# Kernel tuning notes

Hardware: AMD Instinct MI355X
Metric: run time of the kernel (lower is better)

Reference implementation:

```python
import jax, jax.numpy as jnp
import numpy as np

T, V, C, G = 65536, 25, 3, 3
H = 32        # GCN hidden channels
OUT = 8       # cfg.STGCN.OUT_FEATURES
LH = 8        # LSTM hidden
DH = 64       # discriminator hidden


def setup_inputs() -> dict:
    key = jax.random.key(0)
    ks = jax.random.split(key, 16)
    def n(i, shape, s=0.3):
        return jax.random.normal(ks[i], shape, dtype=jnp.float32) * s
    A = jax.random.uniform(ks[0], (V, V), dtype=jnp.float32)
    A = A / A.sum(axis=1, keepdims=True)  # row-normalized adjacency
    return dict(
        x=jax.random.normal(ks[1], (1, C, T, V, G), dtype=jnp.float32),
        x0=jax.random.normal(ks[2], (1, 2), dtype=jnp.float32),
        A=A,
        W1=n(3, (H, C)), b1=jnp.zeros((H,), jnp.float32),
        W2=n(4, (OUT, H)), b2=jnp.zeros((OUT,), jnp.float32),
        Wih0=n(5, (4 * LH, 2)), Whh0=n(6, (4 * LH, LH)),
        bih0=jnp.zeros((4 * LH,), jnp.float32), bhh0=jnp.zeros((4 * LH,), jnp.float32),
        Wih1=n(7, (4 * LH, LH)), Whh1=n(8, (4 * LH, LH)),
        bih1=jnp.zeros((4 * LH,), jnp.float32), bhh1=jnp.zeros((4 * LH,), jnp.float32),
        Wfc1=n(9, (8, 32)), bfc1=jnp.zeros((8,), jnp.float32),
        Wfc2=n(10, (2, 8)), bfc2=jnp.zeros((2,), jnp.float32),
        Wd1=n(11, (DH, 32)), bd1=jnp.zeros((DH,), jnp.float32),
        Wd2=n(12, (1, DH)), bd2=jnp.zeros((1,), jnp.float32),
    )


def reference(x, x0, A, W1, b1, W2, b2,
              Wih0, Whh0, bih0, bhh0, Wih1, Whh1, bih1, bhh1,
              Wfc1, bfc1, Wfc2, bfc2, Wd1, bd1, Wd2, bd2):
    Tn = x.shape[2]
    # --- ST-GCN on every (t, group) slice, vectorized over time ---
    g = jnp.transpose(x[0], (1, 3, 0, 2))                       # [T,G,C,V]
    agg = jnp.einsum('tgcv,vu->tgcu', g, A)                     # graph aggregation
    hid = jax.nn.relu(jnp.einsum('hc,tgcu->tghu', W1, agg)
                      + b1[None, None, :, None])                # [T,G,H,V]
    pooled = hid.mean(axis=-1)                                  # global joint pool [T,G,H]
    gout = (jnp.einsum('oh,tgh->tgo', W2, pooled) + b2).reshape(Tn, G * OUT)  # [T,24]
    # --- circle through the 3 group members (joint 5, channels 0/2), faithful formula ---
    px = x[0, 0, :, 5, :]                                       # [T,3]
    py = x[0, 2, :, 5, :]
    x21 = px[:, 1] - px[:, 0]; y21 = py[:, 1] - py[:, 0]
    x32 = px[:, 2] - px[:, 1]; y32 = py[:, 2] - py[:, 1]
    xy21 = px[:, 1] ** 2 - px[:, 0] ** 2 + py[:, 1] ** 2 - py[:, 0] ** 2
    xy32 = px[:, 2] ** 2 - px[:, 1] ** 2 + py[:, 2] ** 2 - py[:, 1] ** 2
    cy = (x32 * xy21 - x21 * xy32) / 2 * (y21 * x32 - y32 * x21)
    cx = (xy21 - 2 * cy * y21) / (2.0 * x21)
    cr = jnp.sqrt((px[:, 0] - cx) ** 2 + (py[:, 0] - cy) ** 2)

    def lstm_cell(inp, h, c, Wih, Whh, bih, bhh):
        gates = Wih @ inp + bih + Whh @ h + bhh
        i, f, gg, o = jnp.split(gates, 4)
        c2 = jax.nn.sigmoid(f) * c + jax.nn.sigmoid(i) * jnp.tanh(gg)
        return jax.nn.sigmoid(o) * jnp.tanh(c2), c2

    # Re-running the LSTM from zero init over the growing traj and taking the last
    # output (as the torch code does) == stepping the LSTM incrementally.
    def step(carry, xs):
        h0, c0, h1, c1, pt = carry
        go, rx, ry, rr = xs
        h0, c0 = lstm_cell(pt, h0, c0, Wih0, Whh0, bih0, bhh0)
        h1, c1 = lstm_cell(h0, h1, c1, Wih1, Whh1, bih1, bhh1)
        state = jnp.concatenate([h1, go])                       # [32]
        reward = jax.nn.sigmoid(Wd2 @ jnp.tanh(Wd1 @ state + bd1) + bd2)
        nxt = Wfc2 @ (Wfc1 @ state + bfc1) + bfc2               # [2]
        dis = jnp.sqrt((nxt[0] - rx) ** 2 + (nxt[1] - ry) ** 2)
        mask = (dis < rr).astype(jnp.int32)
        return (h0, c0, h1, c1, nxt), (state, nxt, reward, mask)

    z = jnp.zeros((LH,), jnp.float32)
    carry0 = (z, z, z, z, x0.reshape(2))
    xs = (gout[:Tn - 1], cx[:Tn - 1], cy[:Tn - 1], cr[:Tn - 1])
    _, (states, nxts, rewards, masks) = jax.lax.scan(step, carry0, xs)
    traj = jnp.concatenate([x0.reshape(1, 2), nxts], axis=0)    # [T,2]
    return states, traj, rewards, masks
```

## Files before the change

kernel.cpp:

```cpp
#include <hip/hip_runtime.h>
#include <math.h>

#define TT 65536
#define NS 65535
#define VV 25
#define CC 3
#define GG 3
#define HH 32
#define OO 8

#define CHUNK 32
#define NCHUNK 2048
#define WARM 64

#define OFF_WC    0
#define OFF_BC    64
#define OFF_W0H1  128
#define OFF_W1T   384
#define OFF_AT    512
#define OFF_PSCAN 1280

#define OUT_STATES 0
#define OUT_TRAJ   (NS*32)
#define OUT_REW    (OUT_TRAJ + TT*2)
#define OUT_MASK   (OUT_REW + NS)

__device__ __forceinline__ float fsigm(float x){ return 1.0f/(1.0f+__expf(-x)); }
__device__ __forceinline__ float ftanh(float x){ return 2.0f/(1.0f+__expf(-2.0f*x)) - 1.0f; }

#define QP(x, k) __int_as_float(__builtin_amdgcn_update_dpp(0, __float_as_int(x), (k)*0x55, 0xF, 0xF, true))
#define RDL(x, l) __int_as_float(__builtin_amdgcn_readlane(__float_as_int(x), (l)))

__device__ __forceinline__ void pkfma_s(float2& acc, float2 w, float2 h){
  asm("v_pk_fma_f32 %0, %1, %2, %0" : "+v"(acc) : "v"(w), "s"(h));
}
__device__ __forceinline__ void pkmul_s(float2& d, float2 w, float2 h){
  asm("v_pk_mul_f32 %0, %1, %2" : "=v"(d) : "v"(w), "s"(h));
}
__device__ __forceinline__ void pkfma_sv(float2& d, float2 w, float2 p, float2 add){
  asm("v_pk_fma_f32 %0, %1, %2, %3" : "=v"(d) : "v"(w), "s"(p), "v"(add));
}
__device__ __forceinline__ float2 pkadd_v(float2 a, float2 b){
  float2 d; asm("v_pk_add_f32 %0, %1, %2" : "=v"(d) : "v"(a), "v"(b)); return d;
}
__device__ __forceinline__ void pkmul_vv(float2& d, float2 a, float2 b){
  asm("v_pk_mul_f32 %0, %1, %2" : "=v"(d) : "v"(a), "v"(b));
}
__device__ __forceinline__ void pkfma_vv(float2& acc, float2 a, float2 b){
  asm("v_pk_fma_f32 %0, %1, %2, %0" : "+v"(acc) : "v"(a), "v"(b));
}
__device__ __forceinline__ void pkadd_acc(float2& acc, float2 b){
  asm("v_pk_add_f32 %0, %0, %1" : "+v"(acc) : "v"(b));
}

__global__ __launch_bounds__(64) void kW(const float* __restrict__ Wfc1, const float* __restrict__ bfc1,
    const float* __restrict__ Wfc2, const float* __restrict__ bfc2,
    const float* __restrict__ Wih0, const float* __restrict__ x0,
    const float* __restrict__ A, const float* __restrict__ W1, float* __restrict__ ws)
{
  __shared__ float WcL[64];
  int t = threadIdx.x;
  int o = t >> 5, k = t & 31;
  float acc = 0.f;
  #pragma unroll
  for (int m = 0; m < 8; ++m) acc += Wfc2[o*8+m]*Wfc1[m*32+k];
  WcL[t] = acc;
  ws[OFF_WC + t] = acc;
  if (t < 2){
    float b = bfc2[t];
    #pragma unroll
    for (int m = 0; m < 8; ++m) b += Wfc2[t*8+m]*bfc1[m];
    ws[OFF_BC + t] = b;
    ws[OFF_PSCAN + t] = x0[t];
  }
  for (int i = t; i < 26*25; i += 64){
    int u = i / 26, v = i - 26*u;
    ws[OFF_AT + i] = (v < 25) ? A[v*25 + u] : 0.f;
  }
  for (int i = t; i < 96; i += 64){
    int c = i >> 5, h = i & 31;
    ws[OFF_W1T + i] = W1[h*3 + c];
  }
  __syncthreads();
  #pragma unroll
  for (int q = 0; q < 4; ++q){
    int idx = t + 64*q;
    int gg = idx >> 3, jj = idx & 7;
    ws[OFF_W0H1 + idx] = Wih0[gg*2+0]*WcL[jj] + Wih0[gg*2+1]*WcL[32+jj];
  }
}

__global__ __launch_bounds__(192) void kGCN(const float* __restrict__ x,
    const float* __restrict__ b1, const float* __restrict__ W2, const float* __restrict__ b2,
    float* __restrict__ ws, float* __restrict__ out)
{
  __shared__ __align__(16) float smem[192*79];
  __shared__ float goL[192][8];
  const int tid = threadIdx.x;
  const int t0 = blockIdx.x * 64;
  const int dt = tid / 3, g = tid - 3*dt;
  const int t = t0 + dt;

  float2 xp[3][13];
  #pragma unroll
  for (int c = 0; c < CC; ++c){
    if (c) __syncthreads();
    const float4* sc = (const float4*)(x + ((size_t)c*TT + t0)*75);
    float4* dd = (float4*)smem;
    for (int i = tid; i < 1200; i += 192) dd[i] = sc[i];
    __syncthreads();
    const float* bp = smem + dt*75 + g;
    #pragma unroll
    for (int k = 0; k < 12; ++k){ xp[c][k].x = bp[6*k]; xp[c][k].y = bp[6*k+3]; }
    xp[c][12].x = bp[72]; xp[c][12].y = 0.f;
  }
  __syncthreads();

  float* auL = smem + tid*79;
  for (int u = 0; u < VV; ++u){
    const float2* Ap = (const float2*)(ws + OFF_AT + u*26);
    float a24 = ws[OFF_AT + u*26 + 24];
    #pragma unroll
    for (int c = 0; c < CC; ++c){
      float2 acc;
      float2 ap = Ap[0];
      pkmul_vv(acc, xp[c][0], ap);
      #pragma unroll
      for (int k = 1; k < 12; ++k){ float2 apk = Ap[k]; pkfma_vv(acc, xp[c][k], apk); }
      auL[c*26 + u] = __builtin_fmaf(xp[c][12].x, a24, acc.x + acc.y);
    }
  }

  const float2* b1g = (const float2*)b1;
  float2 pooled[16];
  #pragma unroll
  for (int half = 0; half < 2; ++half){
    float2 w1p[3][8], b1p[8], pp[8];
    #pragma unroll
    for (int j = 0; j < 8; ++j){
      b1p[j] = b1g[half*8 + j];
      #pragma unroll
      for (int c = 0; c < 3; ++c)
        w1p[c][j] = *(const float2*)(ws + OFF_W1T + c*32 + half*16 + 2*j);
      pp[j].x = 0.f; pp[j].y = 0.f;
    }
    for (int u = 0; u < VV; ++u){
      float a0 = auL[u], a1 = auL[26 + u], a2 = auL[52 + u];
      float2 a0d; a0d.x = a0; a0d.y = a0;
      float2 a1d; a1d.x = a1; a1d.y = a1;
      float2 a2d; a2d.x = a2; a2d.y = a2;
      #pragma unroll
      for (int j = 0; j < 8; ++j){
        float2 hv = b1p[j];
        pkfma_vv(hv, w1p[0][j], a0d);
        pkfma_vv(hv, w1p[1][j], a1d);
        pkfma_vv(hv, w1p[2][j], a2d);
        hv.x = fmaxf(hv.x, 0.f);
        hv.y = fmaxf(hv.y, 0.f);
        pkadd_acc(pp[j], hv);
      }
    }
    #pragma unroll
    for (int j = 0; j < 8; ++j) pooled[half*8 + j] = pp[j];
  }

  if (t < NS){
    float pm[HH];
    #pragma unroll
    for (int h = 0; h < HH; ++h){
      float ph = (h & 1) ? pooled[h >> 1].y : pooled[h >> 1].x;
      pm[h] = ph * (1.0f/VV);
    }
    #pragma unroll
    for (int o = 0; o < OO; ++o){
      float go = b2[o];
      #pragma unroll
      for (int h = 0; h < HH; ++h) go += W2[o*HH+h]*pm[h];
      out[(size_t)t*32 + 8 + g*8 + o] = go;
      goL[tid][o] = go;
    }
  }
  __syncthreads();

  if (tid < 64){
    int tt = t0 + tid;
    if (tt < NS-1){
      float p0 = ws[OFF_BC+0], p1 = ws[OFF_BC+1];
      #pragma unroll
      for (int k = 0; k < 24; ++k){
        float gk = goL[tid*3 + (k>>3)][k&7];
        p0 += ws[OFF_WC + 8 + k]  * gk;
        p1 += ws[OFF_WC + 40 + k] * gk;
      }
      ws[OFF_PSCAN + 2*(tt+1) + 0] = p0;
      ws[OFF_PSCAN + 2*(tt+1) + 1] = p1;
    }
  }
}

__global__ __launch_bounds__(64) void kScan(const float* __restrict__ ws,
    const float* __restrict__ Wih0, const float* __restrict__ Whh0,
    const float* __restrict__ bih0, const float* __restrict__ bhh0,
    const float* __restrict__ Wih1, const float* __restrict__ Whh1,
    const float* __restrict__ bih1, const float* __restrict__ bhh1,
    float* __restrict__ out)
{
  const int lane = threadIdx.x & 63;
  const int row  = lane & 3;
  const int cell = (lane >> 2) & 7;
  const int G    = row*8 + cell;
  const bool up  = lane >= 32;
  const bool isT = (row == 2);

  const float L2E = 1.4426950408889634f;
  const float nsc = isT ? -2.0f*L2E : -L2E;
  const float k2  = -2.0f*L2E;

  float2 wA[4], wB[4], wP, bP;
  #pragma unroll
  for (int q = 0; q < 4; ++q){
    if (up){
      wA[q].x = nsc*Whh1[G*8 + 2*q];  wA[q].y = nsc*Whh1[G*8 + 2*q+1];
      wB[q].x = nsc*Wih1[G*8 + 2*q];  wB[q].y = nsc*Wih1[G*8 + 2*q+1];
    } else {
      wA[q].x = nsc*ws[OFF_W0H1 + G*8 + 2*q];  wA[q].y = nsc*ws[OFF_W0H1 + G*8 + 2*q+1];
      wB[q].x = nsc*Whh0[G*8 + 2*q];           wB[q].y = nsc*Whh0[G*8 + 2*q+1];
    }
  }
  if (up){ wP.x = 0.f; wP.y = 0.f; bP.x = nsc*(bih1[G] + bhh1[G]); }
  else   { wP.x = nsc*Wih0[G*2+0]; wP.y = nsc*Wih0[G*2+1]; bP.x = nsc*(bih0[G] + bhh0[G]); }
  bP.y = 0.f;

  float cs0 = 0.f, cs1 = 0.f;
  float Dprev = 0.f;
  float2 hp1[4], hp0[4];
  #pragma unroll
  for (int q = 0; q < 4; ++q){ hp1[q].x = 0.f; hp1[q].y = 0.f; hp0[q].x = 0.f; hp0[q].y = 0.f; }

  const float2* Ps = (const float2*)(ws + OFF_PSCAN);
  const bool doStore = up && (row == 0);

  auto STEP = [&](float2 P) -> float {
    float2 accP;
    pkfma_sv(accP, wP, P, bP);
    float2 xa = accP;
    pkfma_s(xa, wA[0], hp1[0]);
    float2 ya;
    pkmul_s(ya, wA[1], hp1[1]);
    pkfma_s(xa, wA[2], hp1[2]);
    pkfma_s(ya, wA[3], hp1[3]);
    float2 sA = pkadd_v(xa, ya);
    float dotA = sA.x + sA.y;
    float gA = dotA + Dprev;

    float e0 = __builtin_amdgcn_exp2f(gA);
    float r0 = __builtin_amdgcn_rcpf(1.0f + e0);
    float iv = QP(r0, 0), fv = QP(r0, 1), gvr = QP(r0, 2), ov = QP(r0, 3);
    float gvc = __builtin_fmaf(gvr, 2.0f*k2, -k2);
    cs0 = __builtin_fmaf(fv, cs0, iv*gvc);
    float ec = __builtin_amdgcn_exp2f(cs0);
    float rc = __builtin_amdgcn_rcpf(1.0f + ec);
    float h0v = __builtin_fmaf(rc, ov + ov, -ov);

    #pragma unroll
    for (int q = 0; q < 4; ++q){ hp0[q].x = RDL(h0v, 8*q); hp0[q].y = RDL(h0v, 8*q + 4); }

    float2 xb, yb;
    pkmul_s(xb, wB[0], hp0[0]);
    pkmul_s(yb, wB[1], hp0[1]);
    pkfma_s(xb, wB[2], hp0[2]);
    pkfma_s(yb, wB[3], hp0[3]);
    float2 sB = pkadd_v(xb, yb);
    float dotB = sB.x + sB.y;
    float gB = dotB + dotA;

    float e1 = __builtin_amdgcn_exp2f(gB);
    float r1 = __builtin_amdgcn_rcpf(1.0f + e1);
    float iw = QP(r1, 0), fw = QP(r1, 1), gwr = QP(r1, 2), ow = QP(r1, 3);
    float gwc = __builtin_fmaf(gwr, 2.0f*k2, -k2);
    cs1 = __builtin_fmaf(fw, cs1, iw*gwc);
    float ed = __builtin_amdgcn_exp2f(cs1);
    float rd = __builtin_amdgcn_rcpf(1.0f + ed);
    float h1v = __builtin_fmaf(rd, ow + ow, -ow);

    #pragma unroll
    for (int q = 0; q < 4; ++q){ hp1[q].x = RDL(h1v, 32 + 8*q); hp1[q].y = RDL(h1v, 32 + 8*q + 4); }

    Dprev = dotB;
    return h1v;
  };

  const int ck   = blockIdx.x;
  const int s0   = ck * CHUNK;
  const int sBeg = (s0 > WARM) ? (s0 - WARM) : 0;
  const int sEnd = (s0 + CHUNK > NS) ? NS : (s0 + CHUNK);
  float* op = out + (size_t)s0*32;

  float2 cur[8], nxt[8];

  if (s0 > sBeg){
    #pragma unroll
    for (int u = 0; u < 8; ++u) cur[u] = Ps[sBeg + u];
    for (int blk = sBeg; blk < s0; blk += 8){
      #pragma unroll
      for (int u = 0; u < 8; ++u){ int ix = blk + 8 + u; nxt[u] = Ps[ix < NS ? ix : NS-1]; }
      #pragma unroll
      for (int u = 0; u < 8; ++u) STEP(cur[u]);
      #pragma unroll
      for (int u = 0; u < 8; ++u) cur[u] = nxt[u];
    }
  }

  {
    const int len   = sEnd - s0;
    const int nfull = len & ~7;
    #pragma unroll
    for (int u = 0; u < 8; ++u){ int ix = s0 + u; cur[u] = Ps[ix < NS ? ix : NS-1]; }
    for (int blk = s0; blk < s0 + nfull; blk += 8){
      #pragma unroll
      for (int u = 0; u < 8; ++u){ int ix = blk + 8 + u; nxt[u] = Ps[ix < NS ? ix : NS-1]; }
      #pragma unroll
      for (int u = 0; u < 8; ++u){
        float h = STEP(cur[u]);
        if (doStore) op[cell] = h;
        op += 32;
      }
      #pragma unroll
      for (int u = 0; u < 8; ++u) cur[u] = nxt[u];
    }
    for (int s = s0 + nfull; s < sEnd; ++s){
      float h = STEP(Ps[s]);
      if (doStore) op[cell] = h;
      op += 32;
    }
  }
}

__global__ __launch_bounds__(256) void kPost(const float* __restrict__ x,
    const float* __restrict__ x0, const float* __restrict__ ws,
    const float* __restrict__ Wd1, const float* __restrict__ bd1,
    const float* __restrict__ Wd2, const float* __restrict__ bd2,
    float* __restrict__ out)
{
  __shared__ float Wd1L[64*32];
  __shared__ float bd1L[64], Wd2L[64], WcLs[64], bcL[2];
  int tid = threadIdx.x;
  for (int i = tid; i < 2048; i += 256) Wd1L[i] = Wd1[i];
  if (tid < 64){ bd1L[tid] = bd1[tid]; Wd2L[tid] = Wd2[tid]; WcLs[tid] = ws[OFF_WC + tid]; }
  if (tid < 2) bcL[tid] = ws[OFF_BC + tid];
  __syncthreads();

  int s = blockIdx.x*256 + tid;
  if (s >= NS) return;

  const float4* rp = (const float4*)(out + (size_t)s*32);
  float st[32];
  #pragma unroll
  for (int q = 0; q < 8; ++q){
    float4 v = rp[q];
    st[4*q] = v.x; st[4*q+1] = v.y; st[4*q+2] = v.z; st[4*q+3] = v.w;
  }
  float n0 = bcL[0], n1 = bcL[1];
  #pragma unroll
  for (int k = 0; k < 32; ++k){ n0 += WcLs[k]*st[k]; n1 += WcLs[32+k]*st[k]; }
  out[OUT_TRAJ + 2*(s+1) + 0] = n0;
  out[OUT_TRAJ + 2*(s+1) + 1] = n1;
  if (s == 0){ out[OUT_TRAJ + 0] = x0[0]; out[OUT_TRAJ + 1] = x0[1]; }

  float accr = bd2[0];
  for (int d = 0; d < 64; ++d){
    float v = bd1L[d];
    #pragma unroll
    for (int k = 0; k < 32; ++k) v += Wd1L[d*32+k]*st[k];
    accr += Wd2L[d]*ftanh(v);
  }
  out[OUT_REW + s] = fsigm(accr);

  float px0 = x[(size_t)s*75 + 15 + 0];
  float px1 = x[(size_t)s*75 + 15 + 1];
  float px2 = x[(size_t)s*75 + 15 + 2];
  const float* py = x + (size_t)2*TT*75;
  float py0 = py[(size_t)s*75 + 15 + 0];
  float py1 = py[(size_t)s*75 + 15 + 1];
  float py2 = py[(size_t)s*75 + 15 + 2];
  float x21 = px1-px0, y21 = py1-py0;
  float x32 = px2-px1, y32 = py2-py1;
  float xy21 = px1*px1 - px0*px0 + py1*py1 - py0*py0;
  float xy32 = px2*px2 - px1*px1 + py2*py2 - py1*py1;
  float cyv = (x32*xy21 - x21*xy32)*0.5f * (y21*x32 - y32*x21);
  float cxv = (xy21 - 2.0f*cyv*y21) / (2.0f*x21);
  float crv = sqrtf((px0-cxv)*(px0-cxv) + (py0-cyv)*(py0-cyv));
  float dx = n0 - cxv, dy = n1 - cyv;
  float dis = sqrtf(dx*dx + dy*dy);
  out[OUT_MASK + s] = (dis < crv) ? 1.0f : 0.0f;
}

extern "C" void kernel_launch(void* const* d_in, const int* in_sizes, int n_in,
                              void* d_out, int out_size, void* d_ws, size_t ws_size,
                              hipStream_t stream) {
  (void)in_sizes; (void)n_in; (void)out_size; (void)ws_size;
  const float* x    = (const float*)d_in[0];
  const float* x0   = (const float*)d_in[1];
  const float* A    = (const float*)d_in[2];
  const float* W1   = (const float*)d_in[3];
  const float* b1   = (const float*)d_in[4];
  const float* W2   = (const float*)d_in[5];
  const float* b2   = (const float*)d_in[6];
  const float* Wih0 = (const float*)d_in[7];
  const float* Whh0 = (const float*)d_in[8];
  const float* bih0 = (const float*)d_in[9];
  const float* bhh0 = (const float*)d_in[10];
  const float* Wih1 = (const float*)d_in[11];
  const float* Whh1 = (const float*)d_in[12];
  const float* bih1 = (const float*)d_in[13];
  const float* bhh1 = (const float*)d_in[14];
  const float* Wfc1 = (const float*)d_in[15];
  const float* bfc1 = (const float*)d_in[16];
  const float* Wfc2 = (const float*)d_in[17];
  const float* bfc2 = (const float*)d_in[18];
  const float* Wd1  = (const float*)d_in[19];
  const float* bd1  = (const float*)d_in[20];
  const float* Wd2  = (const float*)d_in[21];
  const float* bd2  = (const float*)d_in[22];
  float* out = (float*)d_out;
  float* ws  = (float*)d_ws;

  kW   <<<dim3(1),      dim3(64),  0, stream>>>(Wfc1, bfc1, Wfc2, bfc2, Wih0, x0, A, W1, ws);
  kGCN <<<dim3(1024),   dim3(192), 0, stream>>>(x, b1, W2, b2, ws, out);
  kScan<<<dim3(NCHUNK), dim3(64),  0, stream>>>(ws, Wih0, Whh0, bih0, bhh0, Wih1, Whh1, bih1, bhh1, out);
  kPost<<<dim3(256),    dim3(256), 0, stream>>>(x, x0, ws, Wd1, bd1, Wd2, bd2, out);
}
```

Measured before the change: 132.6 us.

## Keep graph aggregation in registers and feed uniform weights as scalar operands

The GCN kernel now computes the graph aggregation one channel at a time, right after each channel's slice is staged. The aggregated values stay in a per-thread register array instead of a large shared-memory scratch area, which shrinks LDS from 192*79 floats to 64*75. The A and W1 weights are passed to packed FMAs as scalar (SGPR) operands, and the joint loops are fully unrolled. This cuts LDS traffic and footprint but raises VGPR pressure, with 75 aggregates held live, which may lower occupancy or cause spills.

```diff
diff --git a/kernel.cpp b/kernel.cpp
--- a/kernel.cpp
+++ b/kernel.cpp
@@ -42,12 +42,6 @@
 }
 __device__ __forceinline__ float2 pkadd_v(float2 a, float2 b){
   float2 d; asm("v_pk_add_f32 %0, %1, %2" : "=v"(d) : "v"(a), "v"(b)); return d;
-}
-__device__ __forceinline__ void pkmul_vv(float2& d, float2 a, float2 b){
-  asm("v_pk_mul_f32 %0, %1, %2" : "=v"(d) : "v"(a), "v"(b));
-}
-__device__ __forceinline__ void pkfma_vv(float2& acc, float2 a, float2 b){
-  asm("v_pk_fma_f32 %0, %1, %2, %0" : "+v"(acc) : "v"(a), "v"(b));
 }
 __device__ __forceinline__ void pkadd_acc(float2& acc, float2 b){
   asm("v_pk_add_f32 %0, %0, %1" : "+v"(acc) : "v"(b));
@@ -94,40 +88,41 @@
     const float* __restrict__ b1, const float* __restrict__ W2, const float* __restrict__ b2,
     float* __restrict__ ws, float* __restrict__ out)
 {
-  __shared__ __align__(16) float smem[192*79];
+  __shared__ __align__(16) float xs[64*75];
   __shared__ float goL[192][8];
   const int tid = threadIdx.x;
   const int t0 = blockIdx.x * 64;
   const int dt = tid / 3, g = tid - 3*dt;
   const int t = t0 + dt;
 
-  float2 xp[3][13];
+  float au[3][25];
+
   #pragma unroll
   for (int c = 0; c < CC; ++c){
     if (c) __syncthreads();
     const float4* sc = (const float4*)(x + ((size_t)c*TT + t0)*75);
-    float4* dd = (float4*)smem;
-    for (int i = tid; i < 1200; i += 192) dd[i] = sc[i];
+    float4* dd = (float4*)xs;
+    #pragma unroll
+    for (int i = 0; i < 7; ++i){
+      int idx = tid + 192*i;
+      if (idx < 1200) dd[idx] = sc[idx];
+    }
     __syncthreads();
-    const float* bp = smem + dt*75 + g;
-    #pragma unroll
-    for (int k = 0; k < 12; ++k){ xp[c][k].x = bp[6*k]; xp[c][k].y = bp[6*k+3]; }
-    xp[c][12].x = bp[72]; xp[c][12].y = 0.f;
-  }
-  __syncthreads();
-
-  float* auL = smem + tid*79;
-  for (int u = 0; u < VV; ++u){
-    const float2* Ap = (const float2*)(ws + OFF_AT + u*26);
-    float a24 = ws[OFF_AT + u*26 + 24];
-    #pragma unroll
-    for (int c = 0; c < CC; ++c){
+    const float* bp = xs + dt*75 + g;
+    float2 xp[13];
+    #pragma unroll
+    for (int k = 0; k < 12; ++k){ xp[k].x = bp[6*k]; xp[k].y = bp[6*k+3]; }
+    xp[12].x = bp[72]; xp[12].y = 0.f;
+
+    #pragma unroll
+    for (int u = 0; u < VV; ++u){
+      const float2* Ap = (const float2*)(ws + OFF_AT + u*26);
+      float a24 = ws[OFF_AT + u*26 + 24];
       float2 acc;
-      float2 ap = Ap[0];
-      pkmul_vv(acc, xp[c][0], ap);
-      #pragma unroll
-      for (int k = 1; k < 12; ++k){ float2 apk = Ap[k]; pkfma_vv(acc, xp[c][k], apk); }
-      auL[c*26 + u] = __builtin_fmaf(xp[c][12].x, a24, acc.x + acc.y);
+      pkmul_s(acc, xp[0], Ap[0]);
+      #pragma unroll
+      for (int k = 1; k < 12; ++k) pkfma_s(acc, xp[k], Ap[k]);
+      au[c][u] = __builtin_fmaf(xp[12].x, a24, acc.x + acc.y);
     }
   }
 
@@ -135,26 +130,26 @@
   float2 pooled[16];
   #pragma unroll
   for (int half = 0; half < 2; ++half){
-    float2 w1p[3][8], b1p[8], pp[8];
+    float2 b1p[8], w1s[3][8], pp[8];
     #pragma unroll
     for (int j = 0; j < 8; ++j){
       b1p[j] = b1g[half*8 + j];
       #pragma unroll
       for (int c = 0; c < 3; ++c)
-        w1p[c][j] = *(const float2*)(ws + OFF_W1T + c*32 + half*16 + 2*j);
+        w1s[c][j] = *(const float2*)(ws + OFF_W1T + c*32 + half*16 + 2*j);
       pp[j].x = 0.f; pp[j].y = 0.f;
     }
+    #pragma unroll
     for (int u = 0; u < VV; ++u){
-      float a0 = auL[u], a1 = auL[26 + u], a2 = auL[52 + u];
-      float2 a0d; a0d.x = a0; a0d.y = a0;
-      float2 a1d; a1d.x = a1; a1d.y = a1;
-      float2 a2d; a2d.x = a2; a2d.y = a2;
+      float2 a0d; a0d.x = au[0][u]; a0d.y = au[0][u];
+      float2 a1d; a1d.x = au[1][u]; a1d.y = au[1][u];
+      float2 a2d; a2d.x = au[2][u]; a2d.y = au[2][u];
       #pragma unroll
       for (int j = 0; j < 8; ++j){
-        float2 hv = b1p[j];
-        pkfma_vv(hv, w1p[0][j], a0d);
-        pkfma_vv(hv, w1p[1][j], a1d);
-        pkfma_vv(hv, w1p[2][j], a2d);
+        float2 hv;
+        pkfma_sv(hv, a0d, w1s[0][j], b1p[j]);
+        pkfma_s(hv, a1d, w1s[1][j]);
+        pkfma_s(hv, a2d, w1s[2][j]);
         hv.x = fmaxf(hv.x, 0.f);
         hv.y = fmaxf(hv.y, 0.f);
         pkadd_acc(pp[j], hv);
```

New measurement: 132.7 us. No clear change (+0.0%).
